# Performance work log

Hardware: AMD Instinct MI355X
Metric: run time of the kernel (lower is better)

## Reference

```python
import jax, jax.numpy as jnp
import numpy as np

B, T, E, H, V = 64, 32, 300, 1024, 10000


def setup_inputs() -> dict:
    key = jax.random.key(0)
    ks = jax.random.split(key, 12)
    s = lambda fan: 1.0 / np.sqrt(fan)
    return {
        "questions": jax.random.randint(ks[0], (B, T), 0, V, dtype=jnp.int64) if jax.config.jax_enable_x64 else jax.random.randint(ks[0], (B, T), 0, V, dtype=jnp.int32),
        "question_lengths": jax.random.randint(ks[1], (B,), 1, T + 1, dtype=jnp.int32),
        "embed_table": jax.random.normal(ks[2], (V, E), jnp.float32) * 0.02,
        "W_ih1": jax.random.normal(ks[3], (4 * H, E), jnp.float32) * s(H),
        "W_hh1": jax.random.normal(ks[4], (4 * H, H), jnp.float32) * s(H),
        "b_ih1": jax.random.normal(ks[5], (4 * H,), jnp.float32) * s(H),
        "b_hh1": jax.random.normal(ks[6], (4 * H,), jnp.float32) * s(H),
        "W_ih2": jax.random.normal(ks[7], (4 * H, H), jnp.float32) * s(H),
        "W_hh2": jax.random.normal(ks[8], (4 * H, H), jnp.float32) * s(H),
        "b_ih2": jax.random.normal(ks[9], (4 * H,), jnp.float32) * s(H),
        "b_hh2": jax.random.normal(ks[10], (4 * H,), jnp.float32) * s(H),
    }


def _lstm_cell(x_t, h, c, W_ih, W_hh, b_ih, b_hh):
    # PyTorch LSTMCell: gate order i, f, g, o
    gates = x_t @ W_ih.T + b_ih + h @ W_hh.T + b_hh  # [B, 4H]
    i, f, g, o = jnp.split(gates, 4, axis=-1)
    c_new = jax.nn.sigmoid(f) * c + jax.nn.sigmoid(i) * jnp.tanh(g)
    h_new = jax.nn.sigmoid(o) * jnp.tanh(c_new)
    return h_new, c_new


def reference(questions, question_lengths, embed_table,
              W_ih1, W_hh1, b_ih1, b_hh1, W_ih2, W_hh2, b_ih2, b_hh2):
    x = embed_table[questions]                      # [B, T, E]
    b, t, _ = x.shape
    h = W_hh1.shape[1]

    def step(carry, inp):
        h1, c1, h2, c2 = carry
        x_t, m = inp                                # x_t [B,E], m [B,1] bool
        h1n, c1n = _lstm_cell(x_t, h1, c1, W_ih1, W_hh1, b_ih1, b_hh1)
        h2n, c2n = _lstm_cell(h1n, h2, c2, W_ih2, W_hh2, b_ih2, b_hh2)
        # samples past their length keep their final state frozen
        h1 = jnp.where(m, h1n, h1); c1 = jnp.where(m, c1n, c1)
        h2 = jnp.where(m, h2n, h2); c2 = jnp.where(m, c2n, c2)
        return (h1, c1, h2, c2), None

    mask = jnp.arange(t)[None, :] < question_lengths[:, None]      # [B,T]
    xs = (jnp.swapaxes(x, 0, 1), jnp.swapaxes(mask, 0, 1)[..., None])
    init = tuple(jnp.zeros((b, h), x.dtype) for _ in range(4))
    (h1, c1, h2, c2), _ = jax.lax.scan(step, init, xs)

    # tile final top-layer hidden to [B, H, 28, 28]
    E_q = jnp.broadcast_to(h2[:, None, None, :], (b, 28, 28, h))
    E_q = jnp.transpose(E_q, (0, 3, 2, 1))
    return (E_q, h1[:, None, :], h2[:, None, :], c1[:, None, :], c2[:, None, :])
```

## Files before the change

### kernel.cpp

```cpp
#include <hip/hip_runtime.h>
#include <hip/hip_bf16.h>
#include <cstdint>

#define B_  64
#define T_  32
#define E_  300
#define EP  320
#define H_  1024
#define G4  4096
#define BH  65536
#define NBLK 192

typedef __attribute__((ext_vector_type(8))) short bf16x8;
typedef __attribute__((ext_vector_type(4))) float f32x4;
typedef unsigned short ushort_t;

__device__ __forceinline__ bf16x8 load_b8(const ushort_t* p) {
    union { uint4 u; bf16x8 v; } c;
    c.u = *reinterpret_cast<const uint4*>(p);
    return c.v;
}

__device__ __forceinline__ ushort_t f2bf(float x) {
    union { float f; uint32_t u; } c; c.f = x;
    uint32_t r = c.u + 0x7fffu + ((c.u >> 16) & 1u);
    return (ushort_t)(r >> 16);
}

__device__ __forceinline__ float sigm(float x) { return 1.0f / (1.0f + __expf(-x)); }

__device__ __forceinline__ void astore64(uint64_t* p, uint64_t v) {
    __hip_atomic_store(p, v, __ATOMIC_RELAXED, __HIP_MEMORY_SCOPE_AGENT);
}
__device__ __forceinline__ uint64_t packf2(float a, float b) {
    union { float f[2]; uint64_t u; } c; c.f[0] = a; c.f[1] = b; return c.u;
}

__device__ __forceinline__ void setflag(int* flags, int role, int js, int val) {
    __hip_atomic_store(&flags[(role * 64 + js) * 16], val,
                       __ATOMIC_RELAXED, __HIP_MEMORY_SCOPE_AGENT);
}
__device__ __forceinline__ void waitwave(const int* flags, int role, int target, int lane) {
    const int* p = &flags[(role * 64 + lane) * 16];
    int guard = 0;
    for (;;) {
        int v = __hip_atomic_load(p, __ATOMIC_RELAXED, __HIP_MEMORY_SCOPE_AGENT);
        if (__all(v >= target)) return;
        if (++guard > (1 << 22)) return;
        __builtin_amdgcn_s_sleep(1);
    }
}

__global__ void prep_inputs(const int* __restrict__ q, const float* __restrict__ table,
                            ushort_t* __restrict__ Xp,
                            const float* __restrict__ Wsrc, ushort_t* __restrict__ Wdst) {
    int blk = blockIdx.x;
    if (blk < 1280) {
        int i = blk * 256 + threadIdx.x;
        const int n = B_ * T_ * EP;
        for (; i < n; i += 1280 * 256) {
            int r = i / EP, c = i - r * EP;
            Xp[i] = (c < E_) ? f2bf(table[q[r] * E_ + c]) : (ushort_t)0;
        }
    } else {
        int i = (blk - 1280) * 256 + threadIdx.x;
        const int n = G4 * EP;
        for (; i < n; i += 2048 * 256) {
            int r = i / EP, c = i - r * EP;
            Wdst[i] = (c < E_) ? f2bf(Wsrc[r * E_ + c]) : (ushort_t)0;
        }
    }
}

__launch_bounds__(256)
__global__ void xgemm(const ushort_t* __restrict__ Xp, const ushort_t* __restrict__ Wp,
                      const float* __restrict__ b_ih1, const float* __restrict__ b_hh1,
                      float* __restrict__ xg) {
    int mblk = blockIdx.x, nblk = blockIdx.y;
    int wave = threadIdx.x >> 6, lane = threadIdx.x & 63;
    int lm = lane & 15, lq = lane >> 4;
    int m0 = mblk * 64 + wave * 16;
    f32x4 acc[4];
    #pragma unroll
    for (int g = 0; g < 4; ++g) {
        int n = nblk * 64 + g * 16 + lm;
        float bv = b_ih1[n] + b_hh1[n];
        acc[g] = (f32x4){bv, bv, bv, bv};
    }
    for (int k0 = 0; k0 < EP; k0 += 32) {
        bf16x8 a = load_b8(Xp + (m0 + lm) * EP + k0 + lq * 8);
        #pragma unroll
        for (int g = 0; g < 4; ++g) {
            bf16x8 b = load_b8(Wp + (nblk * 64 + g * 16 + lm) * EP + k0 + lq * 8);
            acc[g] = __builtin_amdgcn_mfma_f32_16x16x32_bf16(a, b, acc[g], 0, 0, 0);
        }
    }
    #pragma unroll
    for (int g = 0; g < 4; ++g)
        #pragma unroll
        for (int r = 0; r < 4; ++r) {
            int m = m0 + lq * 4 + r;
            int b = m >> 5, t = m & 31;
            int n = nblk * 64 + g * 16 + lm;
            int gate = n >> 10, j = n & 1023;
            xg[(((size_t)t * B_ + b) * H_ + j) * 4 + gate] = acc[g][r];
        }
}


__device__ __forceinline__ void gemm_cm(const ushort_t* __restrict__ hslot,
                                        const ushort_t* __restrict__ wsf,
                                        int lm, int lq, int m0, f32x4 acc[4]) {
    const uint4* hr = reinterpret_cast<const uint4*>(hslot);
    const int rbase = (m0 + lm) * 2 + (lq & 1);
    const int cbo = lq >> 1;
    uint4 buf[32];
    #pragma unroll
    for (int grp = 0; grp < 4; ++grp)
        #pragma unroll
        for (int i = 0; i < 8; ++i)
            buf[grp * 8 + i] = hr[(grp * 16 + i * 2 + cbo) * 128 + rbase];
    #pragma unroll
    for (int grp = 0; grp < 4; ++grp)
        #pragma unroll
        for (int i = 0; i < 8; ++i) {
            int k0 = grp * 256 + i * 32;
            union { uint4 u; bf16x8 v; } a; a.u = buf[grp * 8 + i];
            #pragma unroll
            for (int g = 0; g < 4; ++g) {
                int row = g * 16 + lm;
                bf16x8 bb = load_b8(wsf + row * 1024 + ((k0 + lq * 8) ^ ((lm & 7) << 3)));
                acc[g] = __builtin_amdgcn_mfma_f32_16x16x32_bf16(a.v, bb, acc[g], 0, 0, 0);
            }
        }
}

__device__ __forceinline__ void lstm_elem(const f32x4 acc[4], int r,
                                          float* c, float* h, ushort_t* hb) {
    float iv = sigm(acc[0][r]);
    float fv = sigm(acc[1][r]);
    float gv = tanhf(acc[2][r]);
    float ov = sigm(acc[3][r]);
    float cn = fv * c[r] + iv * gv;
    float hv = ov * tanhf(cn);
    c[r] = cn; h[r] = hv; hb[r] = f2bf(hv);
}

__device__ __forceinline__ void store_h_tile(ushort_t* slot, int js, const ushort_t* hst) {
    int tid = threadIdx.x;
    uint64_t v = reinterpret_cast<const uint64_t*>(hst)[tid];
    astore64(reinterpret_cast<uint64_t*>(slot) + js * 256 + tid, v);
}

__global__ __launch_bounds__(256) void lstm_persist(
    const float* __restrict__ Whh1, const float* __restrict__ Wih2,
    const float* __restrict__ Whh2,
    const float* __restrict__ b_ih2, const float* __restrict__ b_hh2,
    const float* __restrict__ xg, const int* __restrict__ qlen,
    ushort_t* __restrict__ h1hist,
    ushort_t* __restrict__ h2hist,
    float* __restrict__ Qhist,
    float* __restrict__ h1f, float* __restrict__ c1f,
    float* __restrict__ h2f, float* __restrict__ c2f,
    int* __restrict__ flags)
{
    __shared__ ushort_t ws[64 * 1024];
    __shared__ __align__(16) ushort_t hstage[64][16];

    const int blk  = blockIdx.x;
    const int role = blk >> 6;
    const int js   = blk & 63;
    const int wave = threadIdx.x >> 6, lane = threadIdx.x & 63;
    const int lm = lane & 15, lq = lane >> 4;
    const int m0 = wave * 16;

    const float* Wsrc = (role == 0) ? Whh1 : (role == 1) ? Wih2 : Whh2;
    uint2* wsp = reinterpret_cast<uint2*>(ws);
    for (int idx = threadIdx.x; idx < 64 * 256; idx += 256) {
        int r = idx >> 8, c4 = idx & 255;
        int grow = (r >> 4) * H_ + js * 16 + (r & 15);
        float4 v = reinterpret_cast<const float4*>(Wsrc + (size_t)grow * H_)[c4];
        uint2 pk;
        pk.x = (uint32_t)f2bf(v.x) | ((uint32_t)f2bf(v.y) << 16);
        pk.y = (uint32_t)f2bf(v.z) | ((uint32_t)f2bf(v.w) << 16);
        wsp[r * 256 + (c4 ^ ((r & 7) << 1))] = pk;
    }
    __syncthreads();

    int q[4];
    #pragma unroll
    for (int r = 0; r < 4; ++r) q[r] = qlen[m0 + lq * 4 + r];

    float    c_reg[4]  = {0.f, 0.f, 0.f, 0.f};
    float    h_reg[4]  = {0.f, 0.f, 0.f, 0.f};
    ushort_t hb_reg[4] = {0, 0, 0, 0};

    if (role == 0) {
        for (int t = 0; t < T_; ++t) {
            uint4 xq[4];
            #pragma unroll
            for (int r = 0; r < 4; ++r)
                xq[r] = reinterpret_cast<const uint4*>(xg)
                        [((size_t)t * B_ + (m0 + lq * 4 + r)) * H_ + js * 16 + lm];
            if (t > 0) {
                if (wave == 0) waitwave(flags, 0, t, lane);
                __syncthreads();
            }
            f32x4 acc[4];
            #pragma unroll
            for (int r = 0; r < 4; ++r) {
                union { uint32_t u; float f; } x0, x1, x2, x3;
                x0.u = xq[r].x; x1.u = xq[r].y; x2.u = xq[r].z; x3.u = xq[r].w;
                acc[0][r] = x0.f; acc[1][r] = x1.f;
                acc[2][r] = x2.f; acc[3][r] = x3.f;
            }
            gemm_cm(h1hist + (size_t)t * BH, ws, lm, lq, m0, acc);
            #pragma unroll
            for (int r = 0; r < 4; ++r) {
                if (t < q[r]) lstm_elem(acc, r, c_reg, h_reg, hb_reg);
                hstage[m0 + lq * 4 + r][lm] = hb_reg[r];
            }
            __syncthreads();
            store_h_tile(h1hist + (size_t)(t + 1) * BH, js, &hstage[0][0]);
            __syncthreads();
            if (threadIdx.x == 0) setflag(flags, 0, js, t + 1);
        }
        #pragma unroll
        for (int r = 0; r < 4; ++r) {
            int b = m0 + lq * 4 + r, j = js * 16 + lm;
            h1f[b * H_ + j] = h_reg[r]; c1f[b * H_ + j] = c_reg[r];
        }
    } else if (role == 1) {
        float bi[4];
        #pragma unroll
        for (int g = 0; g < 4; ++g) {
            int n = g * H_ + js * 16 + lm;
            bi[g] = b_ih2[n] + b_hh2[n];
        }
        for (int t = 0; t < T_; ++t) {
            if (wave == 0) waitwave(flags, 0, t + 1, lane);
            __syncthreads();
            f32x4 acc[4];
            #pragma unroll
            for (int g = 0; g < 4; ++g) acc[g] = (f32x4){bi[g], bi[g], bi[g], bi[g]};
            gemm_cm(h1hist + (size_t)(t + 1) * BH, ws, lm, lq, m0, acc);
            uint64_t* Qw64 = (uint64_t*)(Qhist + (size_t)t * (4 * BH));
            #pragma unroll
            for (int r = 0; r < 4; ++r) {
                int b = m0 + lq * 4 + r, j = js * 16 + lm;
                size_t base = ((size_t)b * H_ + j) * 2;
                astore64(Qw64 + base,     packf2(acc[0][r], acc[1][r]));
                astore64(Qw64 + base + 1, packf2(acc[2][r], acc[3][r]));
            }
            __syncthreads();
            if (threadIdx.x == 0) setflag(flags, 1, js, t + 1);
        }
    } else {
        for (int t = 0; t < T_; ++t) {
            if (t > 0) {
                if (wave == 0)      waitwave(flags, 1, t + 1, lane);
                else if (wave == 1) waitwave(flags, 2, t,     lane);
            } else {
                if (wave == 0)      waitwave(flags, 1, 1,     lane);
            }
            __syncthreads();
            const uint4* Qr = (const uint4*)(Qhist + (size_t)t * (4 * BH));
            uint4 qp[4];
            #pragma unroll
            for (int r = 0; r < 4; ++r)
                qp[r] = Qr[(size_t)(m0 + lq * 4 + r) * H_ + js * 16 + lm];
            f32x4 acc[4];
            #pragma unroll
            for (int g = 0; g < 4; ++g) acc[g] = (f32x4){0.f, 0.f, 0.f, 0.f};
            gemm_cm(h2hist + (size_t)t * BH, ws, lm, lq, m0, acc);
            #pragma unroll
            for (int r = 0; r < 4; ++r) {
                union { uint32_t u; float f; } x0, x1, x2, x3;
                x0.u = qp[r].x; x1.u = qp[r].y; x2.u = qp[r].z; x3.u = qp[r].w;
                acc[0][r] += x0.f; acc[1][r] += x1.f;
                acc[2][r] += x2.f; acc[3][r] += x3.f;
            }
            #pragma unroll
            for (int r = 0; r < 4; ++r) {
                if (t < q[r]) lstm_elem(acc, r, c_reg, h_reg, hb_reg);
                hstage[m0 + lq * 4 + r][lm] = hb_reg[r];
            }
            __syncthreads();
            store_h_tile(h2hist + (size_t)(t + 1) * BH, js, &hstage[0][0]);
            __syncthreads();
            if (t < T_ - 1 && threadIdx.x == 0) setflag(flags, 2, js, t + 1);
        }
        #pragma unroll
        for (int r = 0; r < 4; ++r) {
            int b = m0 + lq * 4 + r, j = js * 16 + lm;
            h2f[b * H_ + j] = h_reg[r]; c2f[b * H_ + j] = c_reg[r];
        }
    }
}

__global__ void write_out(const float* __restrict__ h1f, const float* __restrict__ h2f,
                          const float* __restrict__ c1f, const float* __restrict__ c2f,
                          float* __restrict__ out) {
    const long long EQ = (long long)B_ * H_ * 784;
    const long long n4 = (EQ + 4LL * B_ * H_) / 4;
    long long i4 = (long long)blockIdx.x * blockDim.x + threadIdx.x;
    long long stride = (long long)gridDim.x * blockDim.x;
    for (; i4 < n4; i4 += stride) {
        long long f = i4 * 4;
        float4 v;
        if (f < EQ) {
            long long bh = f / 784;
            float val = h2f[bh];
            v = make_float4(val, val, val, val);
        } else {
            long long r = f - EQ;
            int which = (int)(r >> 16);
            int j = (int)(r & 65535);
            const float* src = (which == 0) ? h1f : (which == 1) ? h2f : (which == 2) ? c1f : c2f;
            v = *reinterpret_cast<const float4*>(src + j);
        }
        reinterpret_cast<float4*>(out)[i4] = v;
    }
}

extern "C" void kernel_launch(void* const* d_in, const int* in_sizes, int n_in,
                              void* d_out, int out_size, void* d_ws, size_t ws_size,
                              hipStream_t stream) {
    const int*   questions = (const int*)d_in[0];
    const int*   qlen      = (const int*)d_in[1];
    const float* embed     = (const float*)d_in[2];
    const float* W_ih1     = (const float*)d_in[3];
    const float* W_hh1     = (const float*)d_in[4];
    const float* b_ih1     = (const float*)d_in[5];
    const float* b_hh1     = (const float*)d_in[6];
    const float* W_ih2     = (const float*)d_in[7];
    const float* W_hh2     = (const float*)d_in[8];
    const float* b_ih2     = (const float*)d_in[9];
    const float* b_hh2     = (const float*)d_in[10];
    float* out = (float*)d_out;

    char* w = (char*)d_ws;
    float*    xg     = (float*)(w + 0);
    ushort_t* Wih1p  = (ushort_t*)(w + 33554432);
    ushort_t* Xp     = (ushort_t*)(w + 36175872);
    int*      flags  = (int*)(w + 36175872);
    ushort_t* h1hist = (ushort_t*)(w + 37486592);
    ushort_t* h2hist = (ushort_t*)(w + 41811968);
    float*    Qhist  = (float*)(w + 46137344);
    float*    h1f    = (float*)(w + 79691776);
    float*    c1f    = (float*)(w + 79953920);
    float*    h2f    = (float*)(w + 80216064);
    float*    c2f    = (float*)(w + 80478208);

    hipMemsetAsync(w + 37486592, 0, 131072, stream);
    hipMemsetAsync(w + 41811968, 0, 131072, stream);

    prep_inputs<<<3328, 256, 0, stream>>>(questions, embed, Xp, W_ih1, Wih1p);
    xgemm<<<dim3(32, 64), 256, 0, stream>>>(Xp, Wih1p, b_ih1, b_hh1, xg);

    hipMemsetAsync(w + 36175872, 0, 12288, stream);

    lstm_persist<<<NBLK, 256, 0, stream>>>(W_hh1, W_ih2, W_hh2, b_ih2, b_hh2,
                                           xg, qlen,
                                           h1hist, h2hist, Qhist,
                                           h1f, c1f, h2f, c2f, flags);

    write_out<<<4096, 256, 0, stream>>>(h1f, h2f, c1f, c2f, out);
}
```

Baseline: 619.2 us.

## Split recurrent GEMM K dimension across two wave groups per block

Doubles the persistent LSTM block to 512 threads: each of the four M-waves is paired with a second wave that computes the other half of the K=1024 reduction, with partial accumulators combined through shared memory before the gate math. This aims to halve the per-step serial GEMM latency on the recurrence critical path. It adds an extra barrier and an LDS round trip each step. Separately, it folds the two h-slot memsets into the prep kernel as extra zeroing blocks to cut API/launch overhead.

```diff
diff --git a/kernel.cpp b/kernel.cpp
--- a/kernel.cpp
+++ b/kernel.cpp
@@ -53,7 +53,8 @@
 
 __global__ void prep_inputs(const int* __restrict__ q, const float* __restrict__ table,
                             ushort_t* __restrict__ Xp,
-                            const float* __restrict__ Wsrc, ushort_t* __restrict__ Wdst) {
+                            const float* __restrict__ Wsrc, ushort_t* __restrict__ Wdst,
+                            ushort_t* __restrict__ h1s0, ushort_t* __restrict__ h2s0) {
     int blk = blockIdx.x;
     if (blk < 1280) {
         int i = blk * 256 + threadIdx.x;
@@ -62,13 +63,18 @@
             int r = i / EP, c = i - r * EP;
             Xp[i] = (c < E_) ? f2bf(table[q[r] * E_ + c]) : (ushort_t)0;
         }
-    } else {
+    } else if (blk < 3328) {
         int i = (blk - 1280) * 256 + threadIdx.x;
         const int n = G4 * EP;
         for (; i < n; i += 2048 * 256) {
             int r = i / EP, c = i - r * EP;
             Wdst[i] = (c < E_) ? f2bf(Wsrc[r * E_ + c]) : (ushort_t)0;
         }
+    } else {
+        int i = (blk - 3328) * 256 + threadIdx.x;
+        uint4 z = make_uint4(0, 0, 0, 0);
+        if (i < 8192) reinterpret_cast<uint4*>(h1s0)[i] = z;
+        else          reinterpret_cast<uint4*>(h2s0)[i - 8192] = z;
     }
 }
 
@@ -108,23 +114,24 @@
 }
 
 
-__device__ __forceinline__ void gemm_cm(const ushort_t* __restrict__ hslot,
-                                        const ushort_t* __restrict__ wsf,
-                                        int lm, int lq, int m0, f32x4 acc[4]) {
+__device__ __forceinline__ void gemm_half(const ushort_t* __restrict__ hslot,
+                                          const ushort_t* __restrict__ wsf,
+                                          int lm, int lq, int m0, int kh, f32x4 acc[4]) {
     const uint4* hr = reinterpret_cast<const uint4*>(hslot);
     const int rbase = (m0 + lm) * 2 + (lq & 1);
     const int cbo = lq >> 1;
-    uint4 buf[32];
+    const int cb0 = kh * 32;
+    uint4 buf[16];
     #pragma unroll
-    for (int grp = 0; grp < 4; ++grp)
+    for (int grp = 0; grp < 2; ++grp)
         #pragma unroll
         for (int i = 0; i < 8; ++i)
-            buf[grp * 8 + i] = hr[(grp * 16 + i * 2 + cbo) * 128 + rbase];
+            buf[grp * 8 + i] = hr[(cb0 + grp * 16 + i * 2 + cbo) * 128 + rbase];
     #pragma unroll
-    for (int grp = 0; grp < 4; ++grp)
+    for (int grp = 0; grp < 2; ++grp)
         #pragma unroll
         for (int i = 0; i < 8; ++i) {
-            int k0 = grp * 256 + i * 32;
+            int k0 = kh * 512 + grp * 256 + i * 32;
             union { uint4 u; bf16x8 v; } a; a.u = buf[grp * 8 + i];
             #pragma unroll
             for (int g = 0; g < 4; ++g) {
@@ -152,7 +159,7 @@
     astore64(reinterpret_cast<uint64_t*>(slot) + js * 256 + tid, v);
 }
 
-__global__ __launch_bounds__(256) void lstm_persist(
+__global__ __launch_bounds__(512) void lstm_persist(
     const float* __restrict__ Whh1, const float* __restrict__ Wih2,
     const float* __restrict__ Whh2,
     const float* __restrict__ b_ih2, const float* __restrict__ b_hh2,
@@ -166,17 +173,20 @@
 {
     __shared__ ushort_t ws[64 * 1024];
     __shared__ __align__(16) ushort_t hstage[64][16];
+    __shared__ f32x4 pacc[256][4];
 
     const int blk  = blockIdx.x;
     const int role = blk >> 6;
     const int js   = blk & 63;
-    const int wave = threadIdx.x >> 6, lane = threadIdx.x & 63;
+    const int w    = threadIdx.x >> 6, lane = threadIdx.x & 63;
+    const int mi   = w & 3, kh = w >> 2;
     const int lm = lane & 15, lq = lane >> 4;
-    const int m0 = wave * 16;
+    const int m0 = mi * 16;
+    const int pidx = mi * 64 + lane;
 
     const float* Wsrc = (role == 0) ? Whh1 : (role == 1) ? Wih2 : Whh2;
     uint2* wsp = reinterpret_cast<uint2*>(ws);
-    for (int idx = threadIdx.x; idx < 64 * 256; idx += 256) {
+    for (int idx = threadIdx.x; idx < 64 * 256; idx += 512) {
         int r = idx >> 8, c4 = idx & 255;
         int grow = (r >> 4) * H_ + js * 16 + (r & 15);
         float4 v = reinterpret_cast<const float4*>(Wsrc + (size_t)grow * H_)[c4];
@@ -197,38 +207,54 @@
 
     if (role == 0) {
         for (int t = 0; t < T_; ++t) {
-            uint4 xq[4];
-            #pragma unroll
-            for (int r = 0; r < 4; ++r)
-                xq[r] = reinterpret_cast<const uint4*>(xg)
-                        [((size_t)t * B_ + (m0 + lq * 4 + r)) * H_ + js * 16 + lm];
+            f32x4 acc[4];
+            #pragma unroll
+            for (int g = 0; g < 4; ++g) acc[g] = (f32x4){0.f, 0.f, 0.f, 0.f};
+            if (kh == 0) {
+                uint4 xq[4];
+                #pragma unroll
+                for (int r = 0; r < 4; ++r)
+                    xq[r] = reinterpret_cast<const uint4*>(xg)
+                            [((size_t)t * B_ + (m0 + lq * 4 + r)) * H_ + js * 16 + lm];
+                #pragma unroll
+                for (int r = 0; r < 4; ++r) {
+                    union { uint32_t u; float f; } x0, x1, x2, x3;
+                    x0.u = xq[r].x; x1.u = xq[r].y; x2.u = xq[r].z; x3.u = xq[r].w;
+                    acc[0][r] = x0.f; acc[1][r] = x1.f;
+                    acc[2][r] = x2.f; acc[3][r] = x3.f;
+                }
+            }
             if (t > 0) {
-                if (wave == 0) waitwave(flags, 0, t, lane);
+                if (w == 0) waitwave(flags, 0, t, lane);
                 __syncthreads();
             }
-            f32x4 acc[4];
+            gemm_half(h1hist + (size_t)t * BH, ws, lm, lq, m0, kh, acc);
+            if (kh == 1) {
+                #pragma unroll
+                for (int g = 0; g < 4; ++g) pacc[pidx][g] = acc[g];
+            }
+            __syncthreads();
+            if (kh == 0) {
+                #pragma unroll
+                for (int g = 0; g < 4; ++g) acc[g] += pacc[pidx][g];
+                #pragma unroll
+                for (int r = 0; r < 4; ++r) {
+                    if (t < q[r]) lstm_elem(acc, r, c_reg, h_reg, hb_reg);
+                    hstage[m0 + lq * 4 + r][lm] = hb_reg[r];
+                }
+            }
+            __syncthreads();
+            if (threadIdx.x < 256)
+                store_h_tile(h1hist + (size_t)(t + 1) * BH, js, &hstage[0][0]);
+            __syncthreads();
+            if (threadIdx.x == 0) setflag(flags, 0, js, t + 1);
+        }
+        if (kh == 0) {
             #pragma unroll
             for (int r = 0; r < 4; ++r) {
-                union { uint32_t u; float f; } x0, x1, x2, x3;
-                x0.u = xq[r].x; x1.u = xq[r].y; x2.u = xq[r].z; x3.u = xq[r].w;
-                acc[0][r] = x0.f; acc[1][r] = x1.f;
-                acc[2][r] = x2.f; acc[3][r] = x3.f;
-            }
-            gemm_cm(h1hist + (size_t)t * BH, ws, lm, lq, m0, acc);
-            #pragma unroll
-            for (int r = 0; r < 4; ++r) {
-                if (t < q[r]) lstm_elem(acc, r, c_reg, h_reg, hb_reg);
-                hstage[m0 + lq * 4 + r][lm] = hb_reg[r];
-            }
-            __syncthreads();
-            store_h_tile(h1hist + (size_t)(t + 1) * BH, js, &hstage[0][0]);
-            __syncthreads();
-            if (threadIdx.x == 0) setflag(flags, 0, js, t + 1);
-        }
-        #pragma unroll
-        for (int r = 0; r < 4; ++r) {
-            int b = m0 + lq * 4 + r, j = js * 16 + lm;
-            h1f[b * H_ + j] = h_reg[r]; c1f[b * H_ + j] = c_reg[r];
+                int b = m0 + lq * 4 + r, j = js * 16 + lm;
+                h1f[b * H_ + j] = h_reg[r]; c1f[b * H_ + j] = c_reg[r];
+            }
         }
     } else if (role == 1) {
         float bi[4];
@@ -238,62 +264,83 @@
             bi[g] = b_ih2[n] + b_hh2[n];
         }
         for (int t = 0; t < T_; ++t) {
-            if (wave == 0) waitwave(flags, 0, t + 1, lane);
+            if (w == 0) waitwave(flags, 0, t + 1, lane);
             __syncthreads();
             f32x4 acc[4];
             #pragma unroll
-            for (int g = 0; g < 4; ++g) acc[g] = (f32x4){bi[g], bi[g], bi[g], bi[g]};
-            gemm_cm(h1hist + (size_t)(t + 1) * BH, ws, lm, lq, m0, acc);
-            uint64_t* Qw64 = (uint64_t*)(Qhist + (size_t)t * (4 * BH));
+            for (int g = 0; g < 4; ++g)
+                acc[g] = (kh == 0) ? (f32x4){bi[g], bi[g], bi[g], bi[g]}
+                                   : (f32x4){0.f, 0.f, 0.f, 0.f};
+            gemm_half(h1hist + (size_t)(t + 1) * BH, ws, lm, lq, m0, kh, acc);
+            if (kh == 1) {
+                #pragma unroll
+                for (int g = 0; g < 4; ++g) pacc[pidx][g] = acc[g];
+            }
+            __syncthreads();
+            if (kh == 0) {
+                #pragma unroll
+                for (int g = 0; g < 4; ++g) acc[g] += pacc[pidx][g];
+                uint64_t* Qw64 = (uint64_t*)(Qhist + (size_t)t * (4 * BH));
+                #pragma unroll
+                for (int r = 0; r < 4; ++r) {
+                    int b = m0 + lq * 4 + r, j = js * 16 + lm;
+                    size_t base = ((size_t)b * H_ + j) * 2;
+                    astore64(Qw64 + base,     packf2(acc[0][r], acc[1][r]));
+                    astore64(Qw64 + base + 1, packf2(acc[2][r], acc[3][r]));
+                }
+            }
+            __syncthreads();
+            if (threadIdx.x == 0) setflag(flags, 1, js, t + 1);
+        }
+    } else {
+        for (int t = 0; t < T_; ++t) {
+            if (w == 0)               waitwave(flags, 1, t + 1, lane);
+            else if (w == 1 && t > 0) waitwave(flags, 2, t,     lane);
+            __syncthreads();
+            uint4 qp[4];
+            if (kh == 0) {
+                const uint4* Qr = (const uint4*)(Qhist + (size_t)t * (4 * BH));
+                #pragma unroll
+                for (int r = 0; r < 4; ++r)
+                    qp[r] = Qr[(size_t)(m0 + lq * 4 + r) * H_ + js * 16 + lm];
+            }
+            f32x4 acc[4];
+            #pragma unroll
+            for (int g = 0; g < 4; ++g) acc[g] = (f32x4){0.f, 0.f, 0.f, 0.f};
+            gemm_half(h2hist + (size_t)t * BH, ws, lm, lq, m0, kh, acc);
+            if (kh == 1) {
+                #pragma unroll
+                for (int g = 0; g < 4; ++g) pacc[pidx][g] = acc[g];
+            }
+            __syncthreads();
+            if (kh == 0) {
+                #pragma unroll
+                for (int g = 0; g < 4; ++g) acc[g] += pacc[pidx][g];
+                #pragma unroll
+                for (int r = 0; r < 4; ++r) {
+                    union { uint32_t u; float f; } x0, x1, x2, x3;
+                    x0.u = qp[r].x; x1.u = qp[r].y; x2.u = qp[r].z; x3.u = qp[r].w;
+                    acc[0][r] += x0.f; acc[1][r] += x1.f;
+                    acc[2][r] += x2.f; acc[3][r] += x3.f;
+                }
+                #pragma unroll
+                for (int r = 0; r < 4; ++r) {
+                    if (t < q[r]) lstm_elem(acc, r, c_reg, h_reg, hb_reg);
+                    hstage[m0 + lq * 4 + r][lm] = hb_reg[r];
+                }
+            }
+            __syncthreads();
+            if (threadIdx.x < 256)
+                store_h_tile(h2hist + (size_t)(t + 1) * BH, js, &hstage[0][0]);
+            __syncthreads();
+            if (t < T_ - 1 && threadIdx.x == 0) setflag(flags, 2, js, t + 1);
+        }
+        if (kh == 0) {
             #pragma unroll
             for (int r = 0; r < 4; ++r) {
                 int b = m0 + lq * 4 + r, j = js * 16 + lm;
-                size_t base = ((size_t)b * H_ + j) * 2;
-                astore64(Qw64 + base,     packf2(acc[0][r], acc[1][r]));
-                astore64(Qw64 + base + 1, packf2(acc[2][r], acc[3][r]));
-            }
-            __syncthreads();
-            if (threadIdx.x == 0) setflag(flags, 1, js, t + 1);
-        }
-    } else {
-        for (int t = 0; t < T_; ++t) {
-            if (t > 0) {
-                if (wave == 0)      waitwave(flags, 1, t + 1, lane);
-                else if (wave == 1) waitwave(flags, 2, t,     lane);
-            } else {
-                if (wave == 0)      waitwave(flags, 1, 1,     lane);
-            }
-            __syncthreads();
-            const uint4* Qr = (const uint4*)(Qhist + (size_t)t * (4 * BH));
-            uint4 qp[4];
-            #pragma unroll
-            for (int r = 0; r < 4; ++r)
-                qp[r] = Qr[(size_t)(m0 + lq * 4 + r) * H_ + js * 16 + lm];
-            f32x4 acc[4];
-            #pragma unroll
-            for (int g = 0; g < 4; ++g) acc[g] = (f32x4){0.f, 0.f, 0.f, 0.f};
-            gemm_cm(h2hist + (size_t)t * BH, ws, lm, lq, m0, acc);
-            #pragma unroll
-            for (int r = 0; r < 4; ++r) {
-                union { uint32_t u; float f; } x0, x1, x2, x3;
-                x0.u = qp[r].x; x1.u = qp[r].y; x2.u = qp[r].z; x3.u = qp[r].w;
-                acc[0][r] += x0.f; acc[1][r] += x1.f;
-                acc[2][r] += x2.f; acc[3][r] += x3.f;
-            }
-            #pragma unroll
-            for (int r = 0; r < 4; ++r) {
-                if (t < q[r]) lstm_elem(acc, r, c_reg, h_reg, hb_reg);
-                hstage[m0 + lq * 4 + r][lm] = hb_reg[r];
-            }
-            __syncthreads();
-            store_h_tile(h2hist + (size_t)(t + 1) * BH, js, &hstage[0][0]);
-            __syncthreads();
-            if (t < T_ - 1 && threadIdx.x == 0) setflag(flags, 2, js, t + 1);
-        }
-        #pragma unroll
-        for (int r = 0; r < 4; ++r) {
-            int b = m0 + lq * 4 + r, j = js * 16 + lm;
-            h2f[b * H_ + j] = h_reg[r]; c2f[b * H_ + j] = c_reg[r];
+                h2f[b * H_ + j] = h_reg[r]; c2f[b * H_ + j] = c_reg[r];
+            }
         }
     }
 }
@@ -352,15 +399,13 @@
     float*    h2f    = (float*)(w + 80216064);
     float*    c2f    = (float*)(w + 80478208);
 
-    hipMemsetAsync(w + 37486592, 0, 131072, stream);
-    hipMemsetAsync(w + 41811968, 0, 131072, stream);
-
-    prep_inputs<<<3328, 256, 0, stream>>>(questions, embed, Xp, W_ih1, Wih1p);
+    prep_inputs<<<3392, 256, 0, stream>>>(questions, embed, Xp, W_ih1, Wih1p,
+                                          h1hist, h2hist);
     xgemm<<<dim3(32, 64), 256, 0, stream>>>(Xp, Wih1p, b_ih1, b_hh1, xg);
 
     hipMemsetAsync(w + 36175872, 0, 12288, stream);
 
-    lstm_persist<<<NBLK, 256, 0, stream>>>(W_hh1, W_ih2, W_hh2, b_ih2, b_hh2,
+    lstm_persist<<<NBLK, 512, 0, stream>>>(W_hh1, W_ih2, W_hh2, b_ih2, b_hh2,
                                            xg, qlen,
                                            h1hist, h2hist, Qhist,
                                            h1f, c1f, h2f, c2f, flags);
```

New measurement: 529.3 us. -14.5%, faster.
